# Kernel optimization log

Measured on AMD Instinct MI355X. Metric: run time of the kernel, lower is better.

## Reference

```python
import jax, jax.numpy as jnp
import numpy as np

HIDDEN = 1024
N_EXPERTS = 8
TOP_K = 2
INTER = 1408
NORM_TOPK = False


def setup_inputs() -> dict:
    key = jax.random.key(0)
    ks = jax.random.split(key, 5)
    B, S = 4, 2048
    scale_h = 1.0 / np.sqrt(HIDDEN)
    scale_i = 1.0 / np.sqrt(INTER)
    return {
        "hidden_states": jax.random.normal(ks[0], (B, S, HIDDEN), dtype=jnp.float32),
        "gate_w": jax.random.normal(ks[1], (N_EXPERTS, HIDDEN), dtype=jnp.float32) * scale_h,  # router
        "w_gate": jax.random.normal(ks[2], (N_EXPERTS, HIDDEN, INTER), dtype=jnp.float32) * scale_h,
        "w_up": jax.random.normal(ks[3], (N_EXPERTS, HIDDEN, INTER), dtype=jnp.float32) * scale_h,
        "w_down": jax.random.normal(ks[4], (N_EXPERTS, INTER, HIDDEN), dtype=jnp.float32) * scale_i,
    }


def reference(hidden_states, gate_w, w_gate, w_up, w_down):
    B, S, H = hidden_states.shape
    x = hidden_states.reshape(-1, H)                     # [T, H]
    T = x.shape[0]

    router_logits = x @ gate_w.T                          # [T, E]
    probs = jax.nn.softmax(router_logits.astype(jnp.float32), axis=-1)
    topk_w, topk_idx = jax.lax.top_k(probs, TOP_K)        # [T, K]
    if NORM_TOPK:
        topk_w = topk_w / jnp.sum(topk_w, axis=-1, keepdims=True)
    topk_w = topk_w.astype(x.dtype)

    # Scatter top-k weights into dense [T, E] combine weights (0 for unselected).
    weights = jnp.zeros((T, N_EXPERTS), dtype=x.dtype)
    weights = weights.at[jnp.arange(T)[:, None], topk_idx].set(topk_w)

    # Dense grouped SwiGLU over all experts; combine masks out unrouted pairs.
    g = jnp.einsum('th,ehi->eti', x, w_gate)              # [E, T, I]
    u = jnp.einsum('th,ehi->eti', x, w_up)                # [E, T, I]
    y = jnp.einsum('eti,eih->eth', jax.nn.silu(g) * u, w_down)  # [E, T, H]
    final = jnp.einsum('eth,te->th', y, weights)          # [T, H]

    return final.reshape(B, S, H), router_logits
```

## Files before the change

### kernel.cpp

```cpp
#include <hip/hip_runtime.h>
#include <hip/hip_bf16.h>
#include <math.h>

#define T_TOK 8192
#define HID   1024
#define NE    8
#define TOPKN 2
#define INTER 1408
#define NROWS (T_TOK*TOPKN)
#define MAXWL 144
#define MAXWL256 72
#define RBLK  256

typedef __attribute__((ext_vector_type(8))) __bf16 bf16x8;
typedef __attribute__((ext_vector_type(4))) float f32x4;
typedef __attribute__((ext_vector_type(4))) unsigned int u32x4;

__device__ __forceinline__ unsigned short f2bf(float f) {
    unsigned int u = __builtin_bit_cast(unsigned int, f);
    unsigned int lsb = (u >> 16) & 1u;
    u += 0x7fffu + lsb;
    return (unsigned short)(u >> 16);
}

__device__ __forceinline__ void gl2lds16(const void* g, void* l) {
    __builtin_amdgcn_global_load_lds(
        (const __attribute__((address_space(1))) unsigned int*)g,
        (__attribute__((address_space(3))) unsigned int*)l, 16, 0, 0);
}

__global__ __launch_bounds__(256) void moe_router(
    const float* __restrict__ x, const float* __restrict__ gate_w,
    unsigned short* __restrict__ xb, float* __restrict__ logits_out,
    int* __restrict__ topk_idx, float* __restrict__ topk_w,
    int* __restrict__ hist_g)
{
    __shared__ int lh[NE];
    int tid = threadIdx.x, wave = tid >> 6, lane = tid & 63;
    if (tid < NE) lh[tid] = 0;
    __syncthreads();

#pragma unroll 1
    for (int i = 0; i < 8; i++) {
        int t = blockIdx.x * 32 + wave * 8 + i;
        const float4* xr = (const float4*)(x + (size_t)t * HID);
        float acc[NE];
#pragma unroll
        for (int e = 0; e < NE; e++) acc[e] = 0.f;
#pragma unroll
        for (int j = 0; j < 4; j++) {
            float4 xv = xr[j * 64 + lane];
            ushort4 pk;
            pk.x = f2bf(xv.x); pk.y = f2bf(xv.y);
            pk.z = f2bf(xv.z); pk.w = f2bf(xv.w);
            *(ushort4*)(xb + (size_t)t * HID + j * 256 + lane * 4) = pk;
#pragma unroll
            for (int e = 0; e < NE; e++) {
                float4 gv = *(const float4*)(gate_w + e * HID + j * 256 + lane * 4);
                acc[e] += xv.x * gv.x + xv.y * gv.y + xv.z * gv.z + xv.w * gv.w;
            }
        }
#pragma unroll
        for (int e = 0; e < NE; e++) {
            float v = acc[e];
#pragma unroll
            for (int off = 32; off; off >>= 1) v += __shfl_xor(v, off, 64);
            acc[e] = v;
        }
        if (lane == 0) {
            float m = acc[0];
#pragma unroll
            for (int e = 1; e < NE; e++) m = fmaxf(m, acc[e]);
            float p[NE]; float s = 0.f;
#pragma unroll
            for (int e = 0; e < NE; e++) { p[e] = expf(acc[e] - m); s += p[e]; }
            float inv = 1.f / s;
#pragma unroll
            for (int e = 0; e < NE; e++) logits_out[(size_t)t * NE + e] = acc[e];
            int i0 = 0;
#pragma unroll
            for (int e = 1; e < NE; e++) if (p[e] > p[i0]) i0 = e;
            int i1 = (i0 == 0) ? 1 : 0;
#pragma unroll
            for (int e = 0; e < NE; e++) if (e != i0 && p[e] > p[i1]) i1 = e;
            topk_idx[2 * t]     = i0; topk_w[2 * t]     = p[i0] * inv;
            topk_idx[2 * t + 1] = i1; topk_w[2 * t + 1] = p[i1] * inv;
            atomicAdd(&lh[i0], 1);
            atomicAdd(&lh[i1], 1);
        }
    }
    __syncthreads();
    if (tid < NE) hist_g[blockIdx.x * NE + tid] = lh[tid];
}

__global__ __launch_bounds__(256) void moe_scan(
    const int* __restrict__ hist_g, int* __restrict__ offsets,
    int* __restrict__ block_base, int* __restrict__ wl, int* __restrict__ n_wl,
    int* __restrict__ wl256, int* __restrict__ n_wl256)
{
    __shared__ int h[RBLK * NE];
    __shared__ int cnt[NE], offs[NE];
    int tid = threadIdx.x;
    for (int i = tid; i < RBLK * NE; i += 256) h[i] = hist_g[i];
    __syncthreads();
    {
        int e = tid >> 5, g = tid & 31;
        int s = 0;
        for (int b = g; b < RBLK; b += 32) s += h[b * NE + e];
#pragma unroll
        for (int off2 = 16; off2; off2 >>= 1) s += __shfl_xor(s, off2, 32);
        if (g == 0) cnt[e] = s;
    }
    __syncthreads();
    if (tid == 0) {
        int s = 0;
        for (int e = 0; e < NE; e++) { offs[e] = s; offsets[e] = s; s += cnt[e]; }
        offsets[NE] = s;
        int n = 0;
        for (int e = 0; e < NE; e++)
            for (int r0 = 0; r0 < cnt[e]; r0 += 128)
                wl[n++] = (e << 24) | r0;
        *n_wl = n;
        int n2 = 0;
        for (int e = 0; e < NE; e++)
            for (int r0 = 0; r0 < cnt[e]; r0 += 256)
                wl256[n2++] = (e << 24) | r0;
        *n_wl256 = n2;
    }
    __syncthreads();
    if (tid < NE) {
        int run = offs[tid];
        for (int b = 0; b < RBLK; b++) {
            block_base[b * NE + tid] = run;
            run += h[b * NE + tid];
        }
    }
}

__global__ __launch_bounds__(64) void moe_scatter(
    const int* __restrict__ topk_idx, const float* __restrict__ topk_w,
    const int* __restrict__ block_base, int* __restrict__ row_token,
    float* __restrict__ row_w, int* __restrict__ tok_rows)
{
    __shared__ int base[NE];
    int tid = threadIdx.x;
    if (tid < NE) base[tid] = block_base[blockIdx.x * NE + tid];
    __syncthreads();
    int idx = blockIdx.x * 64 + tid;
    int e = topk_idx[idx];
    int pos = atomicAdd(&base[e], 1);
    row_token[pos] = idx >> 1;
    row_w[pos] = topk_w[idx];
    tok_rows[idx] = pos;
}

__global__ __launch_bounds__(256) void moe_transpose_cast(
    const float* __restrict__ in, unsigned short* __restrict__ out,
    int R_, int C_)
{
    __shared__ float tile[64][65];
    int e = blockIdx.z;
    const float* ine = in + (size_t)e * R_ * C_;
    unsigned short* oute = out + (size_t)e * R_ * C_;
    int c0 = blockIdx.x * 64, r0 = blockIdx.y * 64;
    int tid = threadIdx.x;
    int lr = tid >> 4;
    int lc = tid & 15;
#pragma unroll
    for (int j = 0; j < 4; j++) {
        int r = lr + j * 16;
        float4 v = *(const float4*)(ine + (size_t)(r0 + r) * C_ + c0 + lc * 4);
        tile[r][lc * 4 + 0] = v.x; tile[r][lc * 4 + 1] = v.y;
        tile[r][lc * 4 + 2] = v.z; tile[r][lc * 4 + 3] = v.w;
    }
    __syncthreads();
#pragma unroll
    for (int j = 0; j < 4; j++) {
        int c = (tid >> 4) + j * 16;
        int r = (tid & 15) * 4;
        ushort4 pk;
        pk.x = f2bf(tile[r + 0][c]);
        pk.y = f2bf(tile[r + 1][c]);
        pk.z = f2bf(tile[r + 2][c]);
        pk.w = f2bf(tile[r + 3][c]);
        *(ushort4*)(oute + (size_t)(c0 + c) * R_ + r0 + r) = pk;
    }
}

__global__ __launch_bounds__(512, 2) void moe_gemm1(
    const unsigned short* __restrict__ xb,
    const unsigned short* __restrict__ wg_t,
    const unsigned short* __restrict__ wu_t,
    const int* __restrict__ offsets, const int* __restrict__ row_token,
    const int* __restrict__ wl, const int* __restrict__ n_wl,
    unsigned short* __restrict__ h_buf)
{
    if ((int)blockIdx.y >= *n_wl) return;
    int wle = wl[blockIdx.y];
    int e = wle >> 24, row0 = wle & 0xffffff;
    int off = offsets[e], cnt = offsets[e + 1] - off;
    int i0 = blockIdx.x * 128;

    __shared__ __align__(16) unsigned short As[32768];
    __shared__ __align__(16) unsigned short Bs[32768];

    int tid = threadIdx.x, wave = tid >> 6, lane = tid & 63;
    int wm = wave & 1, wn = wave >> 1;
    int l16 = lane & 15, quad = lane >> 4;
    int fsw = (l16 >> 1) & 3;

    int kswz = ((lane & 3) ^ ((lane >> 3) & 3)) * 8;
    int r0s = wave * 32 + (lane >> 2);
    int r1s = r0s + 16;

    int gA0 = row0 + r0s, gA1 = row0 + r1s;
    int tok0 = row_token[off + ((gA0 < cnt) ? gA0 : 0)];
    int tok1 = row_token[off + ((gA1 < cnt) ? gA1 : 0)];
    const unsigned short* aptr0 = xb + (size_t)tok0 * HID + kswz;
    const unsigned short* aptr1 = xb + (size_t)tok1 * HID + kswz;

    int ic0 = i0 + (r0s >> 6) * 32 + (r0s & 31);
    int ic1 = i0 + (r1s >> 6) * 32 + (r1s & 31);
    const unsigned short* bptr0 =
        (((r0s >> 5) & 1) ? wu_t : wg_t) + (size_t)e * INTER * HID + (size_t)ic0 * HID + kswz;
    const unsigned short* bptr1 =
        (((r1s >> 5) & 1) ? wu_t : wg_t) + (size_t)e * INTER * HID + (size_t)ic1 * HID + kswz;

    f32x4 acc[8][4];
#pragma unroll
    for (int mi = 0; mi < 8; mi++)
#pragma unroll
        for (int ni = 0; ni < 4; ni++) acc[mi][ni] = {0.f, 0.f, 0.f, 0.f};

    {
        unsigned short* dA = &As[wave * 1024];
        unsigned short* dB = &Bs[wave * 1024];
        gl2lds16(aptr0, dA);            gl2lds16(aptr1, dA + 512);
        gl2lds16(bptr0, dB);            gl2lds16(bptr1, dB + 512);
        gl2lds16(aptr0 + 32, dA + 8192); gl2lds16(aptr1 + 32, dA + 8192 + 512);
        gl2lds16(bptr0 + 32, dB + 8192); gl2lds16(bptr1 + 32, dB + 8192 + 512);
    }
    __syncthreads();

#pragma unroll 1
    for (int kt = 0; kt < 16; kt++) {
        const unsigned short* Ac = &As[(kt & 1) << 14];
        const unsigned short* Bc = &Bs[(kt & 1) << 14];
        unsigned short* An = &As[(((kt + 1) & 1) << 14) + wave * 1024];
        unsigned short* Bn = &Bs[(((kt + 1) & 1) << 14) + wave * 1024];
        int kb = (kt + 1) * 64;
        bool more = kt < 15;
        bf16x8 a[8], b0, b1;

        asm volatile("s_waitcnt vmcnt(4)" ::: "memory");
        __builtin_amdgcn_s_barrier();
#pragma unroll
        for (int mi = 0; mi < 8; mi++)
            a[mi] = *(const bf16x8*)&Ac[(wm * 128 + mi * 16 + l16) * 32 + (quad ^ fsw) * 8];
        b0 = *(const bf16x8*)&Bc[(wn * 64 + l16) * 32 + (quad ^ fsw) * 8];
        b1 = *(const bf16x8*)&Bc[(wn * 64 + 16 + l16) * 32 + (quad ^ fsw) * 8];
        if (more) { gl2lds16(aptr0 + kb, An); gl2lds16(aptr1 + kb, An + 512); }
        __builtin_amdgcn_s_setprio(1);
#pragma unroll
        for (int mi = 0; mi < 8; mi++) {
            acc[mi][0] = __builtin_amdgcn_mfma_f32_16x16x32_bf16(a[mi], b0, acc[mi][0], 0, 0, 0);
            acc[mi][1] = __builtin_amdgcn_mfma_f32_16x16x32_bf16(a[mi], b1, acc[mi][1], 0, 0, 0);
        }
        __builtin_amdgcn_s_setprio(0);

        asm volatile("s_waitcnt vmcnt(4)" ::: "memory");
        __builtin_amdgcn_s_barrier();
        b0 = *(const bf16x8*)&Bc[(wn * 64 + 32 + l16) * 32 + (quad ^ fsw) * 8];
        b1 = *(const bf16x8*)&Bc[(wn * 64 + 48 + l16) * 32 + (quad ^ fsw) * 8];
        if (more) { gl2lds16(bptr0 + kb, Bn); gl2lds16(bptr1 + kb, Bn + 512); }
        __builtin_amdgcn_s_setprio(1);
#pragma unroll
        for (int mi = 0; mi < 8; mi++) {
            acc[mi][2] = __builtin_amdgcn_mfma_f32_16x16x32_bf16(a[mi], b0, acc[mi][2], 0, 0, 0);
            acc[mi][3] = __builtin_amdgcn_mfma_f32_16x16x32_bf16(a[mi], b1, acc[mi][3], 0, 0, 0);
        }
        __builtin_amdgcn_s_setprio(0);

        asm volatile("s_waitcnt vmcnt(4)" ::: "memory");
        __builtin_amdgcn_s_barrier();
#pragma unroll
        for (int mi = 0; mi < 8; mi++)
            a[mi] = *(const bf16x8*)&Ac[8192 + (wm * 128 + mi * 16 + l16) * 32 + (quad ^ fsw) * 8];
        b0 = *(const bf16x8*)&Bc[8192 + (wn * 64 + l16) * 32 + (quad ^ fsw) * 8];
        b1 = *(const bf16x8*)&Bc[8192 + (wn * 64 + 16 + l16) * 32 + (quad ^ fsw) * 8];
        if (more) { gl2lds16(aptr0 + kb + 32, An + 8192); gl2lds16(aptr1 + kb + 32, An + 8192 + 512); }
        __builtin_amdgcn_s_setprio(1);
#pragma unroll
        for (int mi = 0; mi < 8; mi++) {
            acc[mi][0] = __builtin_amdgcn_mfma_f32_16x16x32_bf16(a[mi], b0, acc[mi][0], 0, 0, 0);
            acc[mi][1] = __builtin_amdgcn_mfma_f32_16x16x32_bf16(a[mi], b1, acc[mi][1], 0, 0, 0);
        }
        __builtin_amdgcn_s_setprio(0);

        asm volatile("s_waitcnt vmcnt(4)" ::: "memory");
        __builtin_amdgcn_s_barrier();
        b0 = *(const bf16x8*)&Bc[8192 + (wn * 64 + 32 + l16) * 32 + (quad ^ fsw) * 8];
        b1 = *(const bf16x8*)&Bc[8192 + (wn * 64 + 48 + l16) * 32 + (quad ^ fsw) * 8];
        if (more) { gl2lds16(bptr0 + kb + 32, Bn + 8192); gl2lds16(bptr1 + kb + 32, Bn + 8192 + 512); }
        __builtin_amdgcn_s_setprio(1);
#pragma unroll
        for (int mi = 0; mi < 8; mi++) {
            acc[mi][2] = __builtin_amdgcn_mfma_f32_16x16x32_bf16(a[mi], b0, acc[mi][2], 0, 0, 0);
            acc[mi][3] = __builtin_amdgcn_mfma_f32_16x16x32_bf16(a[mi], b1, acc[mi][3], 0, 0, 0);
        }
        __builtin_amdgcn_s_setprio(0);
    }

#pragma unroll
    for (int mi = 0; mi < 8; mi++)
#pragma unroll
        for (int np = 0; np < 2; np++)
#pragma unroll
            for (int r = 0; r < 4; r++) {
                int ml = wm * 128 + mi * 16 + quad * 4 + r;
                int row = row0 + ml;
                if (row < cnt) {
                    float g = acc[mi][np][r], u = acc[mi][np + 2][r];
                    float hv = (g / (1.f + expf(-g))) * u;
                    h_buf[(size_t)(off + row) * INTER + i0 + wn * 32 + np * 16 + l16] = f2bf(hv);
                }
            }
}

__global__ __launch_bounds__(256) void moe_gemm2(
    const unsigned short* __restrict__ h_buf,
    const unsigned short* __restrict__ wd_t,
    const int* __restrict__ offsets, const float* __restrict__ row_w,
    const int* __restrict__ wl, const int* __restrict__ n_wl,
    unsigned short* __restrict__ y_buf)
{
    if ((int)blockIdx.y >= *n_wl) return;
    int wle = wl[blockIdx.y];
    int e = wle >> 24, row0 = wle & 0xffffff;
    int off = offsets[e], cnt = offsets[e + 1] - off;
    int h0 = blockIdx.x * 128;

    __shared__ __align__(16) unsigned short As[2][128 * 64];
    __shared__ __align__(16) unsigned short Bs[2][128 * 64];

    int tid = threadIdx.x, wave = tid >> 6, lane = tid & 63;
    int wm = wave & 1, wn = wave >> 1;
    int l16 = lane & 15, quad = lane >> 4;
    int r_ = lane >> 3, c_ = lane & 7;
    int sw = l16 & 7;

    const unsigned short* asrc[4];
    const unsigned short* bsrc[4];
#pragma unroll
    for (int it = 0; it < 4; it++) {
        int rloc = it * 32 + wave * 8 + r_;
        int rg = row0 + rloc;
        asrc[it] = h_buf + (size_t)(off + ((rg < cnt) ? rg : 0)) * INTER + (c_ ^ (rloc & 7)) * 8;
        bsrc[it] = wd_t + (size_t)e * HID * INTER + (size_t)(h0 + rloc) * INTER + (c_ ^ (rloc & 7)) * 8;
    }

    f32x4 acc[4][4];
#pragma unroll
    for (int mi = 0; mi < 4; mi++)
#pragma unroll
        for (int ni = 0; ni < 4; ni++) acc[mi][ni] = {0.f, 0.f, 0.f, 0.f};

    auto stage = [&](unsigned short* asb, unsigned short* bsb, int k0) {
#pragma unroll
        for (int it = 0; it < 4; it++) {
            gl2lds16(asrc[it] + k0, asb + (it * 32 + wave * 8) * 64);
            gl2lds16(bsrc[it] + k0, bsb + (it * 32 + wave * 8) * 64);
        }
    };
    auto compute = [&](const unsigned short* asb, const unsigned short* bsb) {
#pragma unroll
        for (int kk8 = 0; kk8 < 8; kk8 += 4) {
            int q = kk8 + quad;
            int qs = (q ^ sw) * 8;
            bf16x8 a[4], b[4];
#pragma unroll
            for (int mi = 0; mi < 4; mi++)
                a[mi] = *(const bf16x8*)&asb[(wm * 64 + mi * 16 + l16) * 64 + qs];
#pragma unroll
            for (int ni = 0; ni < 4; ni++)
                b[ni] = *(const bf16x8*)&bsb[(wn * 64 + ni * 16 + l16) * 64 + qs];
#pragma unroll
            for (int mi = 0; mi < 4; mi++)
#pragma unroll
                for (int ni = 0; ni < 4; ni++)
                    acc[mi][ni] = __builtin_amdgcn_mfma_f32_16x16x32_bf16(a[mi], b[ni], acc[mi][ni], 0, 0, 0);
        }
    };

    stage(As[0], Bs[0], 0);
    __syncthreads();
#pragma unroll 1
    for (int t = 0; t < 22; t += 2) {
        stage(As[1], Bs[1], (t + 1) * 64);
        compute(As[0], Bs[0]);
        __syncthreads();
        if (t + 2 < 22) stage(As[0], Bs[0], (t + 2) * 64);
        compute(As[1], Bs[1]);
        __syncthreads();
    }

#pragma unroll
    for (int mi = 0; mi < 4; mi++)
#pragma unroll
        for (int ni = 0; ni < 4; ni++)
#pragma unroll
            for (int r = 0; r < 4; r++) {
                int ml = wm * 64 + mi * 16 + quad * 4 + r;
                int row = row0 + ml;
                if (row < cnt) {
                    float w = row_w[off + row];
                    y_buf[(size_t)(off + row) * HID + h0 + wn * 64 + ni * 16 + l16] =
                        f2bf(acc[mi][ni][r] * w);
                }
            }
}

__global__ __launch_bounds__(256) void moe_combine(
    const unsigned short* __restrict__ y_buf, const int* __restrict__ tok_rows,
    float* __restrict__ out)
{
    int gid = blockIdx.x * 256 + threadIdx.x;
    int t = gid >> 7;
    int c = gid & 127;
    u32x4 a = *(const u32x4*)(y_buf + (size_t)tok_rows[2 * t]     * HID + c * 8);
    u32x4 b = *(const u32x4*)(y_buf + (size_t)tok_rows[2 * t + 1] * HID + c * 8);
    float res[8];
#pragma unroll
    for (int j = 0; j < 4; j++) {
        unsigned int wa = a[j], wb = b[j];
        res[2 * j]     = __builtin_bit_cast(float, wa << 16)
                       + __builtin_bit_cast(float, wb << 16);
        res[2 * j + 1] = __builtin_bit_cast(float, wa & 0xffff0000u)
                       + __builtin_bit_cast(float, wb & 0xffff0000u);
    }
    float* o = out + (size_t)t * HID + c * 8;
    *(float4*)(o)     = make_float4(res[0], res[1], res[2], res[3]);
    *(float4*)(o + 4) = make_float4(res[4], res[5], res[6], res[7]);
}

extern "C" void kernel_launch(void* const* d_in, const int* in_sizes, int n_in,
                              void* d_out, int out_size, void* d_ws, size_t ws_size,
                              hipStream_t stream)
{
    const float* x      = (const float*)d_in[0];
    const float* gate_w = (const float*)d_in[1];
    const float* w_gate = (const float*)d_in[2];
    const float* w_up   = (const float*)d_in[3];
    const float* w_down = (const float*)d_in[4];
    float* out = (float*)d_out;
    float* logits_out = out + (size_t)T_TOK * HID;

    char* ws = (char*)d_ws;
    int*   offsets    = (int*)(ws + 0);
    int*   n_wl       = (int*)(ws + 64);
    int*   n_wl256    = (int*)(ws + 68);
    int*   wl         = (int*)(ws + 128);
    int*   wl256      = (int*)(ws + 704);
    int*   hist_g     = (int*)(ws + 1024);
    int*   block_base = (int*)(ws + 1024 + 8192);
    int*   topk_idx   = (int*)(ws + 32768);
    float* topk_w     = (float*)(ws + 32768 + 65536);
    int*   row_token  = (int*)(ws + 32768 + 2 * 65536);
    float* row_w      = (float*)(ws + 32768 + 3 * 65536);
    int*   tok_rows   = (int*)(ws + 32768 + 4 * 65536);
    size_t o = 32768 + 5 * (size_t)65536 + 32768;
    unsigned short* xb   = (unsigned short*)(ws + o); o += (size_t)T_TOK * HID * 2;
    unsigned short* wg_t = (unsigned short*)(ws + o); o += (size_t)NE * INTER * HID * 2;
    unsigned short* wu_t = (unsigned short*)(ws + o); o += (size_t)NE * INTER * HID * 2;
    unsigned short* wd_t = (unsigned short*)(ws + o); o += (size_t)NE * HID * INTER * 2;
    unsigned short* h_buf = (unsigned short*)(ws + o); o += (size_t)NROWS * INTER * 2;
    unsigned short* y_buf = (unsigned short*)(ws + o); o += (size_t)NROWS * HID * 2;

    moe_router<<<RBLK, 256, 0, stream>>>(x, gate_w, xb, logits_out,
                                         topk_idx, topk_w, hist_g);
    moe_scan<<<1, 256, 0, stream>>>(hist_g, offsets, block_base, wl, n_wl,
                                    wl256, n_wl256);
    moe_scatter<<<RBLK, 64, 0, stream>>>(topk_idx, topk_w, block_base,
                                         row_token, row_w, tok_rows);
    moe_transpose_cast<<<dim3(INTER / 64, HID / 64, NE), 256, 0, stream>>>(w_gate, wg_t, HID, INTER);
    moe_transpose_cast<<<dim3(INTER / 64, HID / 64, NE), 256, 0, stream>>>(w_up,   wu_t, HID, INTER);
    moe_transpose_cast<<<dim3(HID / 64, INTER / 64, NE), 256, 0, stream>>>(w_down, wd_t, INTER, HID);

    moe_gemm1<<<dim3(INTER / 128, MAXWL256), 512, 0, stream>>>(
        xb, wg_t, wu_t, offsets, row_token, wl256, n_wl256, h_buf);
    moe_gemm2<<<dim3(HID / 128, MAXWL), 256, 0, stream>>>(
        h_buf, wd_t, offsets, row_w, wl, n_wl, y_buf);
    moe_combine<<<(T_TOK * HID / 8) / 256, 256, 0, stream>>>(y_buf, tok_rows, out);
}
```

Measured before the change: 459.4 us.

## Enlarge down-projection GEMM tile to 256x256 and merge weight transposes

Rewrites the second grouped GEMM to use 256-row by 256-column tiles with 512 threads, reusing the gemm1 pipeline pattern (direct global-to-LDS loads, split A/B staging, priority raising). This gives more data reuse per LDS load and removes the 128-row work list. The three weight transpose-cast launches are merged into one kernel to cut launch overhead. The wait counts in gemm1 are also relaxed to allow more in-flight loads. Larger tiles lower the number of blocks and raise padding waste on partial expert tiles.

```diff
diff --git a/kernel.cpp b/kernel.cpp
--- a/kernel.cpp
+++ b/kernel.cpp
@@ -8,9 +8,10 @@
 #define TOPKN 2
 #define INTER 1408
 #define NROWS (T_TOK*TOPKN)
-#define MAXWL 144
 #define MAXWL256 72
 #define RBLK  256
+#define GX1   (INTER/128)
+#define GX2   (HID/256)
 
 typedef __attribute__((ext_vector_type(8))) __bf16 bf16x8;
 typedef __attribute__((ext_vector_type(4))) float f32x4;
@@ -95,8 +96,7 @@
 
 __global__ __launch_bounds__(256) void moe_scan(
     const int* __restrict__ hist_g, int* __restrict__ offsets,
-    int* __restrict__ block_base, int* __restrict__ wl, int* __restrict__ n_wl,
-    int* __restrict__ wl256, int* __restrict__ n_wl256)
+    int* __restrict__ block_base, int* __restrict__ wl256, int* __restrict__ n_wl256)
 {
     __shared__ int h[RBLK * NE];
     __shared__ int cnt[NE], offs[NE];
@@ -116,11 +116,6 @@
         int s = 0;
         for (int e = 0; e < NE; e++) { offs[e] = s; offsets[e] = s; s += cnt[e]; }
         offsets[NE] = s;
-        int n = 0;
-        for (int e = 0; e < NE; e++)
-            for (int r0 = 0; r0 < cnt[e]; r0 += 128)
-                wl[n++] = (e << 24) | r0;
-        *n_wl = n;
         int n2 = 0;
         for (int e = 0; e < NE; e++)
             for (int r0 = 0; r0 < cnt[e]; r0 += 256)
@@ -154,15 +149,24 @@
     tok_rows[idx] = pos;
 }
 
-__global__ __launch_bounds__(256) void moe_transpose_cast(
-    const float* __restrict__ in, unsigned short* __restrict__ out,
-    int R_, int C_)
+__global__ __launch_bounds__(256) void moe_transpose_all(
+    const float* __restrict__ w_gate, const float* __restrict__ w_up,
+    const float* __restrict__ w_down,
+    unsigned short* __restrict__ wg_t, unsigned short* __restrict__ wu_t,
+    unsigned short* __restrict__ wd_t)
 {
     __shared__ float tile[64][65];
-    int e = blockIdx.z;
+    int z = blockIdx.y;
+    int m = z >> 3, e = z & 7;
+    const float* in; unsigned short* out; int R_, C_;
+    if (m == 0)      { in = w_gate; out = wg_t; R_ = HID;   C_ = INTER; }
+    else if (m == 1) { in = w_up;   out = wu_t; R_ = HID;   C_ = INTER; }
+    else             { in = w_down; out = wd_t; R_ = INTER; C_ = HID;   }
+    int ntx = C_ >> 6;
+    int bx = (int)blockIdx.x % ntx, by = (int)blockIdx.x / ntx;
     const float* ine = in + (size_t)e * R_ * C_;
     unsigned short* oute = out + (size_t)e * R_ * C_;
-    int c0 = blockIdx.x * 64, r0 = blockIdx.y * 64;
+    int c0 = bx * 64, r0 = by * 64;
     int tid = threadIdx.x;
     int lr = tid >> 4;
     int lc = tid & 15;
@@ -268,7 +272,7 @@
         }
         __builtin_amdgcn_s_setprio(0);
 
-        asm volatile("s_waitcnt vmcnt(4)" ::: "memory");
+        asm volatile("s_waitcnt vmcnt(6)" ::: "memory");
         __builtin_amdgcn_s_barrier();
         b0 = *(const bf16x8*)&Bc[(wn * 64 + 32 + l16) * 32 + (quad ^ fsw) * 8];
         b1 = *(const bf16x8*)&Bc[(wn * 64 + 48 + l16) * 32 + (quad ^ fsw) * 8];
@@ -297,7 +301,7 @@
         }
         __builtin_amdgcn_s_setprio(0);
 
-        asm volatile("s_waitcnt vmcnt(4)" ::: "memory");
+        asm volatile("s_waitcnt vmcnt(6)" ::: "memory");
         __builtin_amdgcn_s_barrier();
         b0 = *(const bf16x8*)&Bc[8192 + (wn * 64 + 32 + l16) * 32 + (quad ^ fsw) * 8];
         b1 = *(const bf16x8*)&Bc[8192 + (wn * 64 + 48 + l16) * 32 + (quad ^ fsw) * 8];
@@ -327,7 +331,7 @@
             }
 }
 
-__global__ __launch_bounds__(256) void moe_gemm2(
+__global__ __launch_bounds__(512, 2) void moe_gemm2(
     const unsigned short* __restrict__ h_buf,
     const unsigned short* __restrict__ wd_t,
     const int* __restrict__ offsets, const float* __restrict__ row_w,
@@ -338,79 +342,119 @@
     int wle = wl[blockIdx.y];
     int e = wle >> 24, row0 = wle & 0xffffff;
     int off = offsets[e], cnt = offsets[e + 1] - off;
-    int h0 = blockIdx.x * 128;
-
-    __shared__ __align__(16) unsigned short As[2][128 * 64];
-    __shared__ __align__(16) unsigned short Bs[2][128 * 64];
+    int h0 = blockIdx.x * 256;
+
+    __shared__ __align__(16) unsigned short As[32768];
+    __shared__ __align__(16) unsigned short Bs[32768];
 
     int tid = threadIdx.x, wave = tid >> 6, lane = tid & 63;
     int wm = wave & 1, wn = wave >> 1;
     int l16 = lane & 15, quad = lane >> 4;
-    int r_ = lane >> 3, c_ = lane & 7;
-    int sw = l16 & 7;
-
-    const unsigned short* asrc[4];
-    const unsigned short* bsrc[4];
-#pragma unroll
-    for (int it = 0; it < 4; it++) {
-        int rloc = it * 32 + wave * 8 + r_;
-        int rg = row0 + rloc;
-        asrc[it] = h_buf + (size_t)(off + ((rg < cnt) ? rg : 0)) * INTER + (c_ ^ (rloc & 7)) * 8;
-        bsrc[it] = wd_t + (size_t)e * HID * INTER + (size_t)(h0 + rloc) * INTER + (c_ ^ (rloc & 7)) * 8;
-    }
-
-    f32x4 acc[4][4];
-#pragma unroll
-    for (int mi = 0; mi < 4; mi++)
+    int fsw = (l16 >> 1) & 3;
+
+    int kswz = ((lane & 3) ^ ((lane >> 3) & 3)) * 8;
+    int r0s = wave * 32 + (lane >> 2);
+    int r1s = r0s + 16;
+
+    int gA0 = row0 + r0s, gA1 = row0 + r1s;
+    const unsigned short* aptr0 = h_buf + (size_t)(off + ((gA0 < cnt) ? gA0 : 0)) * INTER + kswz;
+    const unsigned short* aptr1 = h_buf + (size_t)(off + ((gA1 < cnt) ? gA1 : 0)) * INTER + kswz;
+
+    const unsigned short* bptr0 = wd_t + (size_t)e * HID * INTER + (size_t)(h0 + r0s) * INTER + kswz;
+    const unsigned short* bptr1 = wd_t + (size_t)e * HID * INTER + (size_t)(h0 + r1s) * INTER + kswz;
+
+    f32x4 acc[8][4];
+#pragma unroll
+    for (int mi = 0; mi < 8; mi++)
 #pragma unroll
         for (int ni = 0; ni < 4; ni++) acc[mi][ni] = {0.f, 0.f, 0.f, 0.f};
 
-    auto stage = [&](unsigned short* asb, unsigned short* bsb, int k0) {
-#pragma unroll
-        for (int it = 0; it < 4; it++) {
-            gl2lds16(asrc[it] + k0, asb + (it * 32 + wave * 8) * 64);
-            gl2lds16(bsrc[it] + k0, bsb + (it * 32 + wave * 8) * 64);
-        }
-    };
-    auto compute = [&](const unsigned short* asb, const unsigned short* bsb) {
-#pragma unroll
-        for (int kk8 = 0; kk8 < 8; kk8 += 4) {
-            int q = kk8 + quad;
-            int qs = (q ^ sw) * 8;
-            bf16x8 a[4], b[4];
-#pragma unroll
-            for (int mi = 0; mi < 4; mi++)
-                a[mi] = *(const bf16x8*)&asb[(wm * 64 + mi * 16 + l16) * 64 + qs];
-#pragma unroll
-            for (int ni = 0; ni < 4; ni++)
-                b[ni] = *(const bf16x8*)&bsb[(wn * 64 + ni * 16 + l16) * 64 + qs];
-#pragma unroll
-            for (int mi = 0; mi < 4; mi++)
-#pragma unroll
-                for (int ni = 0; ni < 4; ni++)
-                    acc[mi][ni] = __builtin_amdgcn_mfma_f32_16x16x32_bf16(a[mi], b[ni], acc[mi][ni], 0, 0, 0);
-        }
-    };
-
-    stage(As[0], Bs[0], 0);
-    __syncthreads();
+    {
+        unsigned short* dA = &As[wave * 1024];
+        unsigned short* dB = &Bs[wave * 1024];
+        gl2lds16(aptr0, dA);            gl2lds16(aptr1, dA + 512);
+        gl2lds16(bptr0, dB);            gl2lds16(bptr1, dB + 512);
+        gl2lds16(aptr0 + 32, dA + 8192); gl2lds16(aptr1 + 32, dA + 8192 + 512);
+        gl2lds16(bptr0 + 32, dB + 8192); gl2lds16(bptr1 + 32, dB + 8192 + 512);
+    }
+    __syncthreads();
+
 #pragma unroll 1
-    for (int t = 0; t < 22; t += 2) {
-        stage(As[1], Bs[1], (t + 1) * 64);
-        compute(As[0], Bs[0]);
-        __syncthreads();
-        if (t + 2 < 22) stage(As[0], Bs[0], (t + 2) * 64);
-        compute(As[1], Bs[1]);
-        __syncthreads();
-    }
-
-#pragma unroll
-    for (int mi = 0; mi < 4; mi++)
+    for (int kt = 0; kt < 22; kt++) {
+        const unsigned short* Ac = &As[(kt & 1) << 14];
+        const unsigned short* Bc = &Bs[(kt & 1) << 14];
+        unsigned short* An = &As[(((kt + 1) & 1) << 14) + wave * 1024];
+        unsigned short* Bn = &Bs[(((kt + 1) & 1) << 14) + wave * 1024];
+        int kb = (kt + 1) * 64;
+        bool more = kt < 21;
+        bf16x8 a[8], b0, b1;
+
+        asm volatile("s_waitcnt vmcnt(4)" ::: "memory");
+        __builtin_amdgcn_s_barrier();
+#pragma unroll
+        for (int mi = 0; mi < 8; mi++)
+            a[mi] = *(const bf16x8*)&Ac[(wm * 128 + mi * 16 + l16) * 32 + (quad ^ fsw) * 8];
+        b0 = *(const bf16x8*)&Bc[(wn * 64 + l16) * 32 + (quad ^ fsw) * 8];
+        b1 = *(const bf16x8*)&Bc[(wn * 64 + 16 + l16) * 32 + (quad ^ fsw) * 8];
+        if (more) { gl2lds16(aptr0 + kb, An); gl2lds16(aptr1 + kb, An + 512); }
+        __builtin_amdgcn_s_setprio(1);
+#pragma unroll
+        for (int mi = 0; mi < 8; mi++) {
+            acc[mi][0] = __builtin_amdgcn_mfma_f32_16x16x32_bf16(a[mi], b0, acc[mi][0], 0, 0, 0);
+            acc[mi][1] = __builtin_amdgcn_mfma_f32_16x16x32_bf16(a[mi], b1, acc[mi][1], 0, 0, 0);
+        }
+        __builtin_amdgcn_s_setprio(0);
+
+        asm volatile("s_waitcnt vmcnt(6)" ::: "memory");
+        __builtin_amdgcn_s_barrier();
+        b0 = *(const bf16x8*)&Bc[(wn * 64 + 32 + l16) * 32 + (quad ^ fsw) * 8];
+        b1 = *(const bf16x8*)&Bc[(wn * 64 + 48 + l16) * 32 + (quad ^ fsw) * 8];
+        if (more) { gl2lds16(bptr0 + kb, Bn); gl2lds16(bptr1 + kb, Bn + 512); }
+        __builtin_amdgcn_s_setprio(1);
+#pragma unroll
+        for (int mi = 0; mi < 8; mi++) {
+            acc[mi][2] = __builtin_amdgcn_mfma_f32_16x16x32_bf16(a[mi], b0, acc[mi][2], 0, 0, 0);
+            acc[mi][3] = __builtin_amdgcn_mfma_f32_16x16x32_bf16(a[mi], b1, acc[mi][3], 0, 0, 0);
+        }
+        __builtin_amdgcn_s_setprio(0);
+
+        asm volatile("s_waitcnt vmcnt(4)" ::: "memory");
+        __builtin_amdgcn_s_barrier();
+#pragma unroll
+        for (int mi = 0; mi < 8; mi++)
+            a[mi] = *(const bf16x8*)&Ac[8192 + (wm * 128 + mi * 16 + l16) * 32 + (quad ^ fsw) * 8];
+        b0 = *(const bf16x8*)&Bc[8192 + (wn * 64 + l16) * 32 + (quad ^ fsw) * 8];
+        b1 = *(const bf16x8*)&Bc[8192 + (wn * 64 + 16 + l16) * 32 + (quad ^ fsw) * 8];
+        if (more) { gl2lds16(aptr0 + kb + 32, An + 8192); gl2lds16(aptr1 + kb + 32, An + 8192 + 512); }
+        __builtin_amdgcn_s_setprio(1);
+#pragma unroll
+        for (int mi = 0; mi < 8; mi++) {
+            acc[mi][0] = __builtin_amdgcn_mfma_f32_16x16x32_bf16(a[mi], b0, acc[mi][0], 0, 0, 0);
+            acc[mi][1] = __builtin_amdgcn_mfma_f32_16x16x32_bf16(a[mi], b1, acc[mi][1], 0, 0, 0);
+        }
+        __builtin_amdgcn_s_setprio(0);
+
+        asm volatile("s_waitcnt vmcnt(6)" ::: "memory");
+        __builtin_amdgcn_s_barrier();
+        b0 = *(const bf16x8*)&Bc[8192 + (wn * 64 + 32 + l16) * 32 + (quad ^ fsw) * 8];
+        b1 = *(const bf16x8*)&Bc[8192 + (wn * 64 + 48 + l16) * 32 + (quad ^ fsw) * 8];
+        if (more) { gl2lds16(bptr0 + kb + 32, Bn + 8192); gl2lds16(bptr1 + kb + 32, Bn + 8192 + 512); }
+        __builtin_amdgcn_s_setprio(1);
+#pragma unroll
+        for (int mi = 0; mi < 8; mi++) {
+            acc[mi][2] = __builtin_amdgcn_mfma_f32_16x16x32_bf16(a[mi], b0, acc[mi][2], 0, 0, 0);
+            acc[mi][3] = __builtin_amdgcn_mfma_f32_16x16x32_bf16(a[mi], b1, acc[mi][3], 0, 0, 0);
+        }
+        __builtin_amdgcn_s_setprio(0);
+    }
+
+#pragma unroll
+    for (int mi = 0; mi < 8; mi++)
 #pragma unroll
         for (int ni = 0; ni < 4; ni++)
 #pragma unroll
             for (int r = 0; r < 4; r++) {
-                int ml = wm * 64 + mi * 16 + quad * 4 + r;
+                int ml = wm * 128 + mi * 16 + quad * 4 + r;
                 int row = row0 + ml;
                 if (row < cnt) {
                     float w = row_w[off + row];
@@ -457,9 +501,7 @@
 
     char* ws = (char*)d_ws;
     int*   offsets    = (int*)(ws + 0);
-    int*   n_wl       = (int*)(ws + 64);
     int*   n_wl256    = (int*)(ws + 68);
-    int*   wl         = (int*)(ws + 128);
     int*   wl256      = (int*)(ws + 704);
     int*   hist_g     = (int*)(ws + 1024);
     int*   block_base = (int*)(ws + 1024 + 8192);
@@ -478,17 +520,15 @@
 
     moe_router<<<RBLK, 256, 0, stream>>>(x, gate_w, xb, logits_out,
                                          topk_idx, topk_w, hist_g);
-    moe_scan<<<1, 256, 0, stream>>>(hist_g, offsets, block_base, wl, n_wl,
-                                    wl256, n_wl256);
+    moe_scan<<<1, 256, 0, stream>>>(hist_g, offsets, block_base, wl256, n_wl256);
     moe_scatter<<<RBLK, 64, 0, stream>>>(topk_idx, topk_w, block_base,
                                          row_token, row_w, tok_rows);
-    moe_transpose_cast<<<dim3(INTER / 64, HID / 64, NE), 256, 0, stream>>>(w_gate, wg_t, HID, INTER);
-    moe_transpose_cast<<<dim3(INTER / 64, HID / 64, NE), 256, 0, stream>>>(w_up,   wu_t, HID, INTER);
-    moe_transpose_cast<<<dim3(HID / 64, INTER / 64, NE), 256, 0, stream>>>(w_down, wd_t, INTER, HID);
-
-    moe_gemm1<<<dim3(INTER / 128, MAXWL256), 512, 0, stream>>>(
+    moe_transpose_all<<<dim3(352, 24), 256, 0, stream>>>(
+        w_gate, w_up, w_down, wg_t, wu_t, wd_t);
+
+    moe_gemm1<<<dim3(GX1, MAXWL256), 512, 0, stream>>>(
         xb, wg_t, wu_t, offsets, row_token, wl256, n_wl256, h_buf);
-    moe_gemm2<<<dim3(HID / 128, MAXWL), 256, 0, stream>>>(
-        h_buf, wd_t, offsets, row_w, wl, n_wl, y_buf);
+    moe_gemm2<<<dim3(GX2, MAXWL256), 512, 0, stream>>>(
+        h_buf, wd_t, offsets, row_w, wl256, n_wl256, y_buf);
     moe_combine<<<(T_TOK * HID / 8) / 256, 256, 0, stream>>>(y_buf, tok_rows, out);
 }
```

Measured after the change: 443.0 us. 1.04x faster.
